# Performance work log

Hardware: AMD Instinct MI355X
Metric: run time of the kernel (lower is better)

Reference implementation:

```python
import jax, jax.numpy as jnp
import numpy as np

B, NC, F, V, D = 16384, 13, 26, 100000, 16
H1, H2 = 400, 400
DNN_IN = NC + F * D  # 13 + 416 = 429


def setup_inputs() -> dict:
    key = jax.random.key(0)
    ks = jax.random.split(key, 12)
    s = 0.02
    return {
        "continuous": jax.random.normal(ks[0], (B, NC), jnp.float32),
        "cat_idx": jax.random.randint(ks[1], (B, F), 0, V),
        "W_cont": jax.random.normal(ks[2], (NC, 1), jnp.float32) * s,
        "b_cont": jnp.zeros((1,), jnp.float32),
        "emb_first": jax.random.normal(ks[3], (F, V), jnp.float32) * s,
        "emb": jax.random.normal(ks[4], (F, V, D), jnp.float32) * s,
        "W1": jax.random.normal(ks[5], (DNN_IN, H1), jnp.float32) * s,
        "b1": jnp.zeros((H1,), jnp.float32),
        "W2": jax.random.normal(ks[6], (H1, H2), jnp.float32) * s,
        "b2": jnp.zeros((H2,), jnp.float32),
        "W_out": jax.random.normal(ks[7], (H2 + 1, 1), jnp.float32) * s,
        "b_out": jnp.zeros((1,), jnp.float32),
    }


def reference(continuous, cat_idx, W_cont, b_cont, emb_first, emb, W1, b1, W2, b2, W_out, b_out):
    f_ids = jnp.arange(F)  # column ids
    # FM first-order: continuous linear + per-column 1-dim embedding gather, summed over columns
    fm1_cat = emb_first[f_ids[None, :], cat_idx]          # [B, F]
    fm1 = continuous @ W_cont + b_cont + jnp.sum(fm1_cat, axis=1, keepdims=True)  # [B, 1]
    # FM second-order: per-column D-dim embedding gather
    E = emb[f_ids[None, :], cat_idx]                      # [B, F, D]
    sum_emb = jnp.sum(E, axis=1)                          # [B, D]
    fm2 = 0.5 * jnp.sum(sum_emb * sum_emb - jnp.sum(E * E, axis=1), axis=1, keepdims=True)  # [B, 1]
    fm_out = fm1 + fm2
    # DNN on [continuous | flattened embeddings]; Dropout(0.0) is identity
    dnn_in = jnp.concatenate([continuous, E.reshape(E.shape[0], -1)], axis=1)  # [B, 429]
    h = jax.nn.relu(dnn_in @ W1 + b1)
    h = jax.nn.relu(h @ W2 + b2)
    fusion = jnp.concatenate([fm_out, h], axis=1)         # [B, H2+1]
    return fusion @ W_out + b_out                          # [B, 1]
```

## Files before the change

### kernel.cpp

```cpp
#include <hip/hip_runtime.h>
#include <hip/hip_bf16.h>
#include <stdint.h>

#define NB    16384
#define NCONT 13
#define NF    26
#define NV    100000
#define ND    16
#define NH    400
#define K1    448
#define KP1   456
#define K2    416
#define KP2   424
#define NPAD  512
#define ROWS  32

typedef __attribute__((ext_vector_type(8))) __bf16 bf16x8;
typedef __attribute__((ext_vector_type(8))) short short8;
typedef __attribute__((ext_vector_type(4))) float f32x4;

__device__ __forceinline__ short f2bf(float x) {
  union { float f; uint32_t u; } c; c.f = x;
  uint32_t r = (c.u + 0x7FFFu + ((c.u >> 16) & 1u)) >> 16;
  return (short)(uint16_t)r;
}

__global__ __launch_bounds__(256)
void prep_k(const float* __restrict__ W1, const float* __restrict__ W2,
            short* __restrict__ W1T, short* __restrict__ W2T) {
  int t = blockIdx.x * 256 + threadIdx.x;
  if (t < NPAD * K1) {
    int n = t / K1, k = t - n * K1;
    float v = 0.f;
    if (n < NH) {
      if (k < 416)       v = W1[(size_t)(13 + k) * NH + n];
      else if (k < 429)  v = W1[(size_t)(k - 416) * NH + n];
    }
    W1T[t] = f2bf(v);
  } else {
    int u = t - NPAD * K1;
    int n = u / K2, k = u - n * K2;
    float v = (n < NH && k < NH) ? W2[(size_t)k * NH + n] : 0.f;
    W2T[u] = f2bf(v);
  }
}

__global__ __launch_bounds__(256, 2)
void fused_k(const float* __restrict__ cont, const int* __restrict__ cat,
             const float* __restrict__ Wc, const float* __restrict__ bc,
             const float* __restrict__ emb1, const float* __restrict__ emb,
             const short* __restrict__ W1T, const float* __restrict__ b1,
             const short* __restrict__ W2T, const float* __restrict__ b2,
             const float* __restrict__ Wout, const float* __restrict__ bout,
             float* __restrict__ out) {
  __shared__ short lA[ROWS * KP1];
  __shared__ short lH[ROWS * KP2];
  const int tid = threadIdx.x;
  const int bm = blockIdx.x * ROWS;

  {
    const int q  = tid & 7;
    const int rl = tid >> 3;
    const int b  = bm + rl;
    const int f0 = (NF * q) >> 3;
    const int f1 = (NF * (q + 1)) >> 3;
    float se[16];
#pragma unroll
    for (int d = 0; d < 16; d++) se[d] = 0.f;
    float sumsq = 0.f, fm1 = 0.f;

    for (int f = f0; f < f1; f++) {
      int idx = cat[(size_t)b * NF + f];
      const float4* ep = (const float4*)(emb + ((size_t)f * NV + idx) * ND);
      float4 e0 = ep[0], e1 = ep[1], e2 = ep[2], e3 = ep[3];
      fm1 += emb1[(size_t)f * NV + idx];
      se[0] += e0.x; se[1] += e0.y; se[2] += e0.z; se[3] += e0.w;
      se[4] += e1.x; se[5] += e1.y; se[6] += e1.z; se[7] += e1.w;
      se[8] += e2.x; se[9] += e2.y; se[10] += e2.z; se[11] += e2.w;
      se[12] += e3.x; se[13] += e3.y; se[14] += e3.z; se[15] += e3.w;
      sumsq += e0.x*e0.x + e0.y*e0.y + e0.z*e0.z + e0.w*e0.w
             + e1.x*e1.x + e1.y*e1.y + e1.z*e1.z + e1.w*e1.w
             + e2.x*e2.x + e2.y*e2.y + e2.z*e2.z + e2.w*e2.w
             + e3.x*e3.x + e3.y*e3.y + e3.z*e3.z + e3.w*e3.w;
      short8 p0, p1;
      p0[0]=f2bf(e0.x); p0[1]=f2bf(e0.y); p0[2]=f2bf(e0.z); p0[3]=f2bf(e0.w);
      p0[4]=f2bf(e1.x); p0[5]=f2bf(e1.y); p0[6]=f2bf(e1.z); p0[7]=f2bf(e1.w);
      p1[0]=f2bf(e2.x); p1[1]=f2bf(e2.y); p1[2]=f2bf(e2.z); p1[3]=f2bf(e2.w);
      p1[4]=f2bf(e3.x); p1[5]=f2bf(e3.y); p1[6]=f2bf(e3.z); p1[7]=f2bf(e3.w);
      *(short8*)&lA[rl * KP1 + f * 16]     = p0;
      *(short8*)&lA[rl * KP1 + f * 16 + 8] = p1;
    }
#pragma unroll
    for (int d = 0; d < 16; d++) {
      se[d] += __shfl_xor(se[d], 1, 64);
      se[d] += __shfl_xor(se[d], 2, 64);
      se[d] += __shfl_xor(se[d], 4, 64);
    }
    sumsq += __shfl_xor(sumsq, 1, 64);
    sumsq += __shfl_xor(sumsq, 2, 64);
    sumsq += __shfl_xor(sumsq, 4, 64);
    fm1   += __shfl_xor(fm1, 1, 64);
    fm1   += __shfl_xor(fm1, 2, 64);
    fm1   += __shfl_xor(fm1, 4, 64);

    if (q == 0) {
      float s2 = 0.f;
#pragma unroll
      for (int d = 0; d < 16; d++) s2 += se[d] * se[d];
      float fm2 = 0.5f * (s2 - sumsq);
      float fmc = bc[0];
      short tail[32];
#pragma unroll
      for (int i = 0; i < NCONT; i++) {
        float c = cont[(size_t)b * NCONT + i];
        fmc += c * Wc[i];
        tail[i] = f2bf(c);
      }
#pragma unroll
      for (int i = NCONT; i < 32; i++) tail[i] = 0;
#pragma unroll
      for (int v = 0; v < 4; v++) {
        short8 tv;
#pragma unroll
        for (int e = 0; e < 8; e++) tv[e] = tail[v * 8 + e];
        *(short8*)&lA[rl * KP1 + 416 + v * 8] = tv;
      }
      out[b] = (fm1 + fmc + fm2) * Wout[0] + bout[0];
    }
  }
  __syncthreads();

  const int lane = tid & 63;
  const int wave = tid >> 6;
  const int lrow = lane & 15;
  const int quad = lane >> 4;
  const int wn   = wave * 128;
  const int kq   = quad * 8;
  f32x4 acc[2][8];

#pragma unroll
  for (int i = 0; i < 2; i++)
#pragma unroll
    for (int j = 0; j < 8; j++)
#pragma unroll
      for (int r = 0; r < 4; r++) acc[i][j][r] = 0.f;
  {
    const short* wp[8];
#pragma unroll
    for (int j = 0; j < 8; j++)
      wp[j] = W1T + (size_t)(wn + j * 16 + lrow) * K1 + kq;
    bf16x8 wf[2][8], af[2][2];
#pragma unroll
    for (int j = 0; j < 8; j++) wf[0][j] = *(const bf16x8*)(wp[j]);
#pragma unroll
    for (int i = 0; i < 2; i++) af[0][i] = *(const bf16x8*)&lA[(i * 16 + lrow) * KP1 + kq];
#pragma unroll
    for (int ks = 0; ks < K1 / 32; ks++) {
      const int cur = ks & 1, nxt = cur ^ 1;
      if (ks + 1 < K1 / 32) {
#pragma unroll
        for (int j = 0; j < 8; j++) wf[nxt][j] = *(const bf16x8*)(wp[j] + (ks + 1) * 32);
#pragma unroll
        for (int i = 0; i < 2; i++)
          af[nxt][i] = *(const bf16x8*)&lA[(i * 16 + lrow) * KP1 + (ks + 1) * 32 + kq];
      }
#pragma unroll
      for (int i = 0; i < 2; i++)
#pragma unroll
        for (int j = 0; j < 8; j++)
          acc[i][j] = __builtin_amdgcn_mfma_f32_16x16x32_bf16(af[cur][i], wf[cur][j], acc[i][j], 0, 0, 0);
    }
  }
#pragma unroll
  for (int j = 0; j < 8; j++) {
    int col = wn + j * 16 + lrow;
    if (col < K2) {
      float bias = (col < NH) ? b1[col] : 0.f;
#pragma unroll
      for (int i = 0; i < 2; i++)
#pragma unroll
        for (int r = 0; r < 4; r++) {
          int row = i * 16 + quad * 4 + r;
          float v = (col < NH) ? fmaxf(acc[i][j][r] + bias, 0.f) : 0.f;
          lH[row * KP2 + col] = f2bf(v);
        }
    }
  }
  __syncthreads();

#pragma unroll
  for (int i = 0; i < 2; i++)
#pragma unroll
    for (int j = 0; j < 8; j++)
#pragma unroll
      for (int r = 0; r < 4; r++) acc[i][j][r] = 0.f;
  {
    const short* wp[8];
#pragma unroll
    for (int j = 0; j < 8; j++)
      wp[j] = W2T + (size_t)(wn + j * 16 + lrow) * K2 + kq;
    bf16x8 wf[2][8], af[2][2];
#pragma unroll
    for (int j = 0; j < 8; j++) wf[0][j] = *(const bf16x8*)(wp[j]);
#pragma unroll
    for (int i = 0; i < 2; i++) af[0][i] = *(const bf16x8*)&lH[(i * 16 + lrow) * KP2 + kq];
#pragma unroll
    for (int ks = 0; ks < K2 / 32; ks++) {
      const int cur = ks & 1, nxt = cur ^ 1;
      if (ks + 1 < K2 / 32) {
#pragma unroll
        for (int j = 0; j < 8; j++) wf[nxt][j] = *(const bf16x8*)(wp[j] + (ks + 1) * 32);
#pragma unroll
        for (int i = 0; i < 2; i++)
          af[nxt][i] = *(const bf16x8*)&lH[(i * 16 + lrow) * KP2 + (ks + 1) * 32 + kq];
      }
#pragma unroll
      for (int i = 0; i < 2; i++)
#pragma unroll
        for (int j = 0; j < 8; j++)
          acc[i][j] = __builtin_amdgcn_mfma_f32_16x16x32_bf16(af[cur][i], wf[cur][j], acc[i][j], 0, 0, 0);
    }
  }
  {
    float bw[8], wo[8];
#pragma unroll
    for (int j = 0; j < 8; j++) {
      int col = wn + j * 16 + lrow;
      bw[j] = (col < NH) ? b2[col] : 0.f;
      wo[j] = (col < NH) ? Wout[1 + col] : 0.f;
    }
#pragma unroll
    for (int i = 0; i < 2; i++) {
#pragma unroll
      for (int r = 0; r < 4; r++) {
        float s = 0.f;
#pragma unroll
        for (int j = 0; j < 8; j++)
          s += fmaxf(acc[i][j][r] + bw[j], 0.f) * wo[j];
        s += __shfl_xor(s, 1, 64);
        s += __shfl_xor(s, 2, 64);
        s += __shfl_xor(s, 4, 64);
        s += __shfl_xor(s, 8, 64);
        if (lrow == 0) atomicAdd(&out[bm + i * 16 + quad * 4 + r], s);
      }
    }
  }
}

extern "C" void kernel_launch(void* const* d_in, const int* in_sizes, int n_in,
                              void* d_out, int out_size, void* d_ws, size_t ws_size,
                              hipStream_t stream) {
  const float* cont   = (const float*)d_in[0];
  const int*   cat    = (const int*)d_in[1];
  const float* W_cont = (const float*)d_in[2];
  const float* b_cont = (const float*)d_in[3];
  const float* emb1   = (const float*)d_in[4];
  const float* emb    = (const float*)d_in[5];
  const float* W1     = (const float*)d_in[6];
  const float* b1     = (const float*)d_in[7];
  const float* W2     = (const float*)d_in[8];
  const float* b2     = (const float*)d_in[9];
  const float* W_out  = (const float*)d_in[10];
  const float* b_out  = (const float*)d_in[11];
  float* out = (float*)d_out;

  char* ws = (char*)d_ws;
  short* W1T = (short*)ws;
  short* W2T = (short*)(ws + (size_t)NPAD * K1 * 2);
  (void)ws_size; (void)in_sizes; (void)n_in; (void)out_size;

  prep_k<<<dim3((NPAD * K1 + NPAD * K2) / 256), dim3(256), 0, stream>>>(W1, W2, W1T, W2T);
  fused_k<<<dim3(NB / ROWS), dim3(256), 0, stream>>>(cont, cat, W_cont, b_cont,
                                                     emb1, emb, W1T, b1, W2T, b2,
                                                     W_out, b_out, out);
}
```

Before: 281.4 us.

## Split embedding gather into separate kernel and trim padded MLP columns

```diff
diff --git a/kernel.cpp b/kernel.cpp
--- a/kernel.cpp
+++ b/kernel.cpp
@@ -12,7 +12,8 @@
 #define KP1   456
 #define K2    416
 #define KP2   424
-#define NPAD  512
+#define NPAD  448
+#define NJ    7
 #define ROWS  32
 
 typedef __attribute__((ext_vector_type(8))) __bf16 bf16x8;
@@ -45,88 +46,131 @@
   }
 }
 
+__global__ __launch_bounds__(256)
+void gather_k(const float* __restrict__ cont, const int* __restrict__ cat,
+              const float* __restrict__ Wc, const float* __restrict__ bc,
+              const float* __restrict__ emb1, const float* __restrict__ emb,
+              const float* __restrict__ Wout, const float* __restrict__ bout,
+              short* __restrict__ dnn, float* __restrict__ out) {
+  const int t = blockIdx.x * 256 + threadIdx.x;
+  const int b = t >> 3;
+  const int q = t & 7;
+  float se[16];
+#pragma unroll
+  for (int d = 0; d < 16; d++) se[d] = 0.f;
+  float sumsq = 0.f, fm1 = 0.f;
+  short* drow = dnn + (size_t)b * K1;
+
+#pragma unroll
+  for (int fi = 0; fi < 4; fi++) {
+    const int f = q + 8 * fi;
+    if (fi == 3 && q >= 2) break;
+    int idx = cat[(size_t)b * NF + f];
+    const float4* ep = (const float4*)(emb + ((size_t)f * NV + idx) * ND);
+    float4 e0 = ep[0], e1 = ep[1], e2 = ep[2], e3 = ep[3];
+    fm1 += emb1[(size_t)f * NV + idx];
+    se[0] += e0.x; se[1] += e0.y; se[2] += e0.z; se[3] += e0.w;
+    se[4] += e1.x; se[5] += e1.y; se[6] += e1.z; se[7] += e1.w;
+    se[8] += e2.x; se[9] += e2.y; se[10] += e2.z; se[11] += e2.w;
+    se[12] += e3.x; se[13] += e3.y; se[14] += e3.z; se[15] += e3.w;
+    sumsq += e0.x*e0.x + e0.y*e0.y + e0.z*e0.z + e0.w*e0.w
+           + e1.x*e1.x + e1.y*e1.y + e1.z*e1.z + e1.w*e1.w
+           + e2.x*e2.x + e2.y*e2.y + e2.z*e2.z + e2.w*e2.w
+           + e3.x*e3.x + e3.y*e3.y + e3.z*e3.z + e3.w*e3.w;
+    short8 p0, p1;
+    p0[0]=f2bf(e0.x); p0[1]=f2bf(e0.y); p0[2]=f2bf(e0.z); p0[3]=f2bf(e0.w);
+    p0[4]=f2bf(e1.x); p0[5]=f2bf(e1.y); p0[6]=f2bf(e1.z); p0[7]=f2bf(e1.w);
+    p1[0]=f2bf(e2.x); p1[1]=f2bf(e2.y); p1[2]=f2bf(e2.z); p1[3]=f2bf(e2.w);
+    p1[4]=f2bf(e3.x); p1[5]=f2bf(e3.y); p1[6]=f2bf(e3.z); p1[7]=f2bf(e3.w);
+    *(short8*)(drow + f * 16)     = p0;
+    *(short8*)(drow + f * 16 + 8) = p1;
+  }
+#pragma unroll
+  for (int d = 0; d < 16; d++) {
+    se[d] += __shfl_xor(se[d], 1, 64);
+    se[d] += __shfl_xor(se[d], 2, 64);
+    se[d] += __shfl_xor(se[d], 4, 64);
+  }
+  sumsq += __shfl_xor(sumsq, 1, 64);
+  sumsq += __shfl_xor(sumsq, 2, 64);
+  sumsq += __shfl_xor(sumsq, 4, 64);
+  fm1   += __shfl_xor(fm1, 1, 64);
+  fm1   += __shfl_xor(fm1, 2, 64);
+  fm1   += __shfl_xor(fm1, 4, 64);
+
+  if (q == 0) {
+    float s2 = 0.f;
+#pragma unroll
+    for (int d = 0; d < 16; d++) s2 += se[d] * se[d];
+    float fm2 = 0.5f * (s2 - sumsq);
+    float fmc = bc[0];
+    short tail[32];
+#pragma unroll
+    for (int i = 0; i < NCONT; i++) {
+      float c = cont[(size_t)b * NCONT + i];
+      fmc += c * Wc[i];
+      tail[i] = f2bf(c);
+    }
+#pragma unroll
+    for (int i = NCONT; i < 32; i++) tail[i] = 0;
+#pragma unroll
+    for (int v = 0; v < 4; v++) {
+      short8 tv;
+#pragma unroll
+      for (int e = 0; e < 8; e++) tv[e] = tail[v * 8 + e];
+      *(short8*)(drow + 416 + v * 8) = tv;
+    }
+    out[b] = (fm1 + fmc + fm2) * Wout[0] + bout[0];
+  }
+}
+
+template <int K, int KP>
+__device__ __forceinline__ void layer(const short* __restrict__ WT, const short* lds,
+                                      int wave, int lrow, int kq, f32x4 acc[2][NJ]) {
+  const short* wp[NJ];
+#pragma unroll
+  for (int j = 0; j < NJ; j++)
+    wp[j] = WT + (size_t)((wave + 4 * j) * 16 + lrow) * K + kq;
+  bf16x8 wf[2][NJ], af[2][2];
+#pragma unroll
+  for (int j = 0; j < NJ; j++) wf[0][j] = *(const bf16x8*)(wp[j]);
+#pragma unroll
+  for (int i = 0; i < 2; i++) af[0][i] = *(const bf16x8*)(lds + (i * 16 + lrow) * KP + kq);
+#pragma unroll
+  for (int ks = 0; ks < K / 32; ks++) {
+    const int cur = ks & 1, nxt = cur ^ 1;
+    if (ks + 1 < K / 32) {
+#pragma unroll
+      for (int j = 0; j < NJ; j++) wf[nxt][j] = *(const bf16x8*)(wp[j] + (ks + 1) * 32);
+#pragma unroll
+      for (int i = 0; i < 2; i++)
+        af[nxt][i] = *(const bf16x8*)(lds + (i * 16 + lrow) * KP + (ks + 1) * 32 + kq);
+    }
+#pragma unroll
+    for (int i = 0; i < 2; i++)
+#pragma unroll
+      for (int j = 0; j < NJ; j++)
+        acc[i][j] = __builtin_amdgcn_mfma_f32_16x16x32_bf16(af[cur][i], wf[cur][j], acc[i][j], 0, 0, 0);
+  }
+}
+
 __global__ __launch_bounds__(256, 2)
-void fused_k(const float* __restrict__ cont, const int* __restrict__ cat,
-             const float* __restrict__ Wc, const float* __restrict__ bc,
-             const float* __restrict__ emb1, const float* __restrict__ emb,
-             const short* __restrict__ W1T, const float* __restrict__ b1,
-             const short* __restrict__ W2T, const float* __restrict__ b2,
-             const float* __restrict__ Wout, const float* __restrict__ bout,
-             float* __restrict__ out) {
+void dnn_k(const short* __restrict__ dnn,
+           const short* __restrict__ W1T, const float* __restrict__ b1,
+           const short* __restrict__ W2T, const float* __restrict__ b2,
+           const float* __restrict__ Wout, float* __restrict__ out) {
   __shared__ short lA[ROWS * KP1];
   __shared__ short lH[ROWS * KP2];
   const int tid = threadIdx.x;
   const int bm = blockIdx.x * ROWS;
 
   {
-    const int q  = tid & 7;
-    const int rl = tid >> 3;
-    const int b  = bm + rl;
-    const int f0 = (NF * q) >> 3;
-    const int f1 = (NF * (q + 1)) >> 3;
-    float se[16];
-#pragma unroll
-    for (int d = 0; d < 16; d++) se[d] = 0.f;
-    float sumsq = 0.f, fm1 = 0.f;
-
-    for (int f = f0; f < f1; f++) {
-      int idx = cat[(size_t)b * NF + f];
-      const float4* ep = (const float4*)(emb + ((size_t)f * NV + idx) * ND);
-      float4 e0 = ep[0], e1 = ep[1], e2 = ep[2], e3 = ep[3];
-      fm1 += emb1[(size_t)f * NV + idx];
-      se[0] += e0.x; se[1] += e0.y; se[2] += e0.z; se[3] += e0.w;
-      se[4] += e1.x; se[5] += e1.y; se[6] += e1.z; se[7] += e1.w;
-      se[8] += e2.x; se[9] += e2.y; se[10] += e2.z; se[11] += e2.w;
-      se[12] += e3.x; se[13] += e3.y; se[14] += e3.z; se[15] += e3.w;
-      sumsq += e0.x*e0.x + e0.y*e0.y + e0.z*e0.z + e0.w*e0.w
-             + e1.x*e1.x + e1.y*e1.y + e1.z*e1.z + e1.w*e1.w
-             + e2.x*e2.x + e2.y*e2.y + e2.z*e2.z + e2.w*e2.w
-             + e3.x*e3.x + e3.y*e3.y + e3.z*e3.z + e3.w*e3.w;
-      short8 p0, p1;
-      p0[0]=f2bf(e0.x); p0[1]=f2bf(e0.y); p0[2]=f2bf(e0.z); p0[3]=f2bf(e0.w);
-      p0[4]=f2bf(e1.x); p0[5]=f2bf(e1.y); p0[6]=f2bf(e1.z); p0[7]=f2bf(e1.w);
-      p1[0]=f2bf(e2.x); p1[1]=f2bf(e2.y); p1[2]=f2bf(e2.z); p1[3]=f2bf(e2.w);
-      p1[4]=f2bf(e3.x); p1[5]=f2bf(e3.y); p1[6]=f2bf(e3.z); p1[7]=f2bf(e3.w);
-      *(short8*)&lA[rl * KP1 + f * 16]     = p0;
-      *(short8*)&lA[rl * KP1 + f * 16 + 8] = p1;
-    }
-#pragma unroll
-    for (int d = 0; d < 16; d++) {
-      se[d] += __shfl_xor(se[d], 1, 64);
-      se[d] += __shfl_xor(se[d], 2, 64);
-      se[d] += __shfl_xor(se[d], 4, 64);
-    }
-    sumsq += __shfl_xor(sumsq, 1, 64);
-    sumsq += __shfl_xor(sumsq, 2, 64);
-    sumsq += __shfl_xor(sumsq, 4, 64);
-    fm1   += __shfl_xor(fm1, 1, 64);
-    fm1   += __shfl_xor(fm1, 2, 64);
-    fm1   += __shfl_xor(fm1, 4, 64);
-
-    if (q == 0) {
-      float s2 = 0.f;
-#pragma unroll
-      for (int d = 0; d < 16; d++) s2 += se[d] * se[d];
-      float fm2 = 0.5f * (s2 - sumsq);
-      float fmc = bc[0];
-      short tail[32];
-#pragma unroll
-      for (int i = 0; i < NCONT; i++) {
-        float c = cont[(size_t)b * NCONT + i];
-        fmc += c * Wc[i];
-        tail[i] = f2bf(c);
-      }
-#pragma unroll
-      for (int i = NCONT; i < 32; i++) tail[i] = 0;
-#pragma unroll
-      for (int v = 0; v < 4; v++) {
-        short8 tv;
-#pragma unroll
-        for (int e = 0; e < 8; e++) tv[e] = tail[v * 8 + e];
-        *(short8*)&lA[rl * KP1 + 416 + v * 8] = tv;
-      }
-      out[b] = (fm1 + fmc + fm2) * Wout[0] + bout[0];
-    }
+    const int r = tid >> 3, s = (tid & 7) * 56;
+    const short* g = dnn + (size_t)(bm + r) * K1 + s;
+    short* l = &lA[r * KP1 + s];
+#pragma unroll
+    for (int c = 0; c < 7; c++)
+      *(short8*)(l + c * 8) = *(const short8*)(g + c * 8);
   }
   __syncthreads();
 
@@ -134,46 +178,20 @@
   const int wave = tid >> 6;
   const int lrow = lane & 15;
   const int quad = lane >> 4;
-  const int wn   = wave * 128;
   const int kq   = quad * 8;
-  f32x4 acc[2][8];
+  f32x4 acc[2][NJ];
 
 #pragma unroll
   for (int i = 0; i < 2; i++)
 #pragma unroll
-    for (int j = 0; j < 8; j++)
+    for (int j = 0; j < NJ; j++)
 #pragma unroll
       for (int r = 0; r < 4; r++) acc[i][j][r] = 0.f;
-  {
-    const short* wp[8];
-#pragma unroll
-    for (int j = 0; j < 8; j++)
-      wp[j] = W1T + (size_t)(wn + j * 16 + lrow) * K1 + kq;
-    bf16x8 wf[2][8], af[2][2];
-#pragma unroll
-    for (int j = 0; j < 8; j++) wf[0][j] = *(const bf16x8*)(wp[j]);
-#pragma unroll
-    for (int i = 0; i < 2; i++) af[0][i] = *(const bf16x8*)&lA[(i * 16 + lrow) * KP1 + kq];
-#pragma unroll
-    for (int ks = 0; ks < K1 / 32; ks++) {
-      const int cur = ks & 1, nxt = cur ^ 1;
-      if (ks + 1 < K1 / 32) {
-#pragma unroll
-        for (int j = 0; j < 8; j++) wf[nxt][j] = *(const bf16x8*)(wp[j] + (ks + 1) * 32);
-#pragma unroll
-        for (int i = 0; i < 2; i++)
-          af[nxt][i] = *(const bf16x8*)&lA[(i * 16 + lrow) * KP1 + (ks + 1) * 32 + kq];
-      }
-#pragma unroll
-      for (int i = 0; i < 2; i++)
-#pragma unroll
-        for (int j = 0; j < 8; j++)
-          acc[i][j] = __builtin_amdgcn_mfma_f32_16x16x32_bf16(af[cur][i], wf[cur][j], acc[i][j], 0, 0, 0);
-    }
-  }
-#pragma unroll
-  for (int j = 0; j < 8; j++) {
-    int col = wn + j * 16 + lrow;
+  layer<K1, KP1>(W1T, lA, wave, lrow, kq, acc);
+
+#pragma unroll
+  for (int j = 0; j < NJ; j++) {
+    int col = (wave + 4 * j) * 16 + lrow;
     if (col < K2) {
       float bias = (col < NH) ? b1[col] : 0.f;
 #pragma unroll
@@ -191,41 +209,16 @@
 #pragma unroll
   for (int i = 0; i < 2; i++)
 #pragma unroll
-    for (int j = 0; j < 8; j++)
+    for (int j = 0; j < NJ; j++)
 #pragma unroll
       for (int r = 0; r < 4; r++) acc[i][j][r] = 0.f;
+  layer<K2, KP2>(W2T, lH, wave, lrow, kq, acc);
+
   {
-    const short* wp[8];
-#pragma unroll
-    for (int j = 0; j < 8; j++)
-      wp[j] = W2T + (size_t)(wn + j * 16 + lrow) * K2 + kq;
-    bf16x8 wf[2][8], af[2][2];
-#pragma unroll
-    for (int j = 0; j < 8; j++) wf[0][j] = *(const bf16x8*)(wp[j]);
-#pragma unroll
-    for (int i = 0; i < 2; i++) af[0][i] = *(const bf16x8*)&lH[(i * 16 + lrow) * KP2 + kq];
-#pragma unroll
-    for (int ks = 0; ks < K2 / 32; ks++) {
-      const int cur = ks & 1, nxt = cur ^ 1;
-      if (ks + 1 < K2 / 32) {
-#pragma unroll
-        for (int j = 0; j < 8; j++) wf[nxt][j] = *(const bf16x8*)(wp[j] + (ks + 1) * 32);
-#pragma unroll
-        for (int i = 0; i < 2; i++)
-          af[nxt][i] = *(const bf16x8*)&lH[(i * 16 + lrow) * KP2 + (ks + 1) * 32 + kq];
-      }
-#pragma unroll
-      for (int i = 0; i < 2; i++)
-#pragma unroll
-        for (int j = 0; j < 8; j++)
-          acc[i][j] = __builtin_amdgcn_mfma_f32_16x16x32_bf16(af[cur][i], wf[cur][j], acc[i][j], 0, 0, 0);
-    }
-  }
-  {
-    float bw[8], wo[8];
-#pragma unroll
-    for (int j = 0; j < 8; j++) {
-      int col = wn + j * 16 + lrow;
+    float bw[NJ], wo[NJ];
+#pragma unroll
+    for (int j = 0; j < NJ; j++) {
+      int col = (wave + 4 * j) * 16 + lrow;
       bw[j] = (col < NH) ? b2[col] : 0.f;
       wo[j] = (col < NH) ? Wout[1 + col] : 0.f;
     }
@@ -235,7 +228,7 @@
       for (int r = 0; r < 4; r++) {
         float s = 0.f;
 #pragma unroll
-        for (int j = 0; j < 8; j++)
+        for (int j = 0; j < NJ; j++)
           s += fmaxf(acc[i][j][r] + bw[j], 0.f) * wo[j];
         s += __shfl_xor(s, 1, 64);
         s += __shfl_xor(s, 2, 64);
@@ -265,12 +258,14 @@
   float* out = (float*)d_out;
 
   char* ws = (char*)d_ws;
-  short* W1T = (short*)ws;
-  short* W2T = (short*)(ws + (size_t)NPAD * K1 * 2);
+  size_t off = 0;
+  short* dnn = (short*)(ws + off); off += (size_t)NB * K1 * 2;
+  short* W1T = (short*)(ws + off); off += (size_t)NPAD * K1 * 2;
+  short* W2T = (short*)(ws + off); off += (size_t)NPAD * K2 * 2;
   (void)ws_size; (void)in_sizes; (void)n_in; (void)out_size;
 
   prep_k<<<dim3((NPAD * K1 + NPAD * K2) / 256), dim3(256), 0, stream>>>(W1, W2, W1T, W2T);
-  fused_k<<<dim3(NB / ROWS), dim3(256), 0, stream>>>(cont, cat, W_cont, b_cont,
-                                                     emb1, emb, W1T, b1, W2T, b2,
-                                                     W_out, b_out, out);
-}
+  gather_k<<<dim3(NB * 8 / 256), dim3(256), 0, stream>>>(cont, cat, W_cont, b_cont,
+                                                         emb1, emb, W_out, b_out, dnn, out);
+  dnn_k<<<dim3(NB / ROWS), dim3(256), 0, stream>>>(dnn, W1T, b1, W2T, b2, W_out, out);
+}
```

New measurement: 285.5 us. No clear change (+1.4%).
